# Performance work log

Hardware: AMD Instinct MI355X
Metric: run time of the kernel (lower is better)

The kernel has to match this reference:

```python
import jax, jax.numpy as jnp
import numpy as np

H = 16        # num_attention_heads
G = 16        # groups
SCALE_MIN = 0.95
SCALE_MAX = 1.05


def setup_inputs() -> dict:
    key = jax.random.key(0)
    ks = jax.random.split(key, 9)
    B, S, E = 2, 2048, 1024
    d = {
        'hidden_states': jax.random.normal(ks[0], (B, S, E), jnp.float32),
        'Wq': jax.random.normal(ks[1], (E, E), jnp.float32) * (E ** -0.5),
        'bq': jax.random.normal(ks[2], (E,), jnp.float32) * 0.02,
        'Wk': jax.random.normal(ks[3], (E, E), jnp.float32) * (E ** -0.5),
        'bk': jax.random.normal(ks[4], (E,), jnp.float32) * 0.02,
        'Wv': jax.random.normal(ks[5], (E, E), jnp.float32) * (E ** -0.5),
        'bv': jax.random.normal(ks[6], (E,), jnp.float32) * 0.02,
        'Ws': jax.random.normal(ks[7], (H * G, E), jnp.float32) * (E ** -0.5),
        'bs': jax.random.normal(ks[8], (H * G,), jnp.float32) * 0.02,
    }
    return d


def _shape_heads(x, B, S):
    # [B,S,h*D] -> [B,h,S,D]
    return x.reshape(B, S, H, -1).transpose(0, 2, 1, 3)


def reference(hidden_states, Wq, bq, Wk, bk, Wv, bv, Ws, bs):
    B, S, E = hidden_states.shape
    D = E // H            # head dim = 64
    gd = D // G           # group dim = 4

    Q = _shape_heads(hidden_states @ Wq.T + bq, B, S)   # [B,h,S,D]
    K = _shape_heads(hidden_states @ Wk.T + bk, B, S)
    V = _shape_heads(hidden_states @ Wv.T + bv, B, S)

    # groupwise dynamic scales, narrow sigmoid range
    s_logits = hidden_states @ Ws.T + bs                 # [B,S,h*g]
    s = jax.nn.sigmoid(s_logits) * (SCALE_MAX - SCALE_MIN) + SCALE_MIN
    s = s.reshape(B, S, H, G).transpose(0, 2, 1, 3)      # [B,h,S,g]
    s = jnp.repeat(s, gd, axis=-1)                       # [B,h,S,D]

    Q = Q * s  # apply_to='q'

    scores = jnp.einsum('bhsd,bhtd->bhst', Q, K) / jnp.sqrt(jnp.float32(D))
    probs = jax.nn.softmax(scores, axis=-1)
    ctx = jnp.einsum('bhst,bhtd->bhsd', probs, V)        # [B,h,S,D]
    ctx = ctx.transpose(0, 2, 1, 3).reshape(B, S, H * D)
    return ctx
```

## Files before the change

### kernel.cpp

```cpp
#include <hip/hip_runtime.h>

typedef short bf16x8 __attribute__((ext_vector_type(8)));
typedef short bf16x4 __attribute__((ext_vector_type(4)));
typedef float f32x4 __attribute__((ext_vector_type(4)));

__device__ inline float bf2f(ushort u) {
    unsigned v = ((unsigned)u) << 16;
    return __builtin_bit_cast(float, v);
}
__device__ inline ushort f2bf(float f) {
    unsigned u = __builtin_bit_cast(unsigned, f);
    u += 0x7fffu + ((u >> 16) & 1u);
    return (ushort)(u >> 16);
}
__device__ inline void async_load16(const ushort* g, ushort* l) {
    __builtin_amdgcn_global_load_lds((const __attribute__((address_space(1))) void*)g,
                                     (__attribute__((address_space(3))) void*)l, 16, 0, 0);
}
__device__ inline f32x4 mfma16(bf16x4 a, bf16x4 b, f32x4 c) {
#if __has_builtin(__builtin_amdgcn_mfma_f32_16x16x16_bf16)
    return __builtin_amdgcn_mfma_f32_16x16x16_bf16(a, b, c, 0, 0, 0);
#else
    return __builtin_amdgcn_mfma_f32_16x16x16bf16_1k(a, b, c, 0, 0, 0);
#endif
}

__global__ void cast_all(const float* __restrict__ hs, const float* __restrict__ Wq,
                         const float* __restrict__ Wk, const float* __restrict__ Wv,
                         const float* __restrict__ Ws,
                         ushort* __restrict__ dhs, ushort* __restrict__ dWq,
                         ushort* __restrict__ dWk, ushort* __restrict__ dWv,
                         ushort* __restrict__ dWs)
{
    int bid = blockIdx.x;
    const float* src; ushort* dst; int off;
    if (bid < 2048)      { src = hs; dst = dhs; off = bid; }
    else if (bid < 2560) { src = Wq; dst = dWq; off = bid - 2048; }
    else if (bid < 3072) { src = Wk; dst = dWk; off = bid - 2560; }
    else if (bid < 3584) { src = Wv; dst = dWv; off = bid - 3072; }
    else                 { src = Ws; dst = dWs; off = bid - 3584; }
    int i = (off * 256 + threadIdx.x) * 8;
    float4 a = *(const float4*)(src + i);
    float4 b = *(const float4*)(src + i + 4);
    union { ushort u[8]; float4 v; } o;
    o.u[0] = f2bf(a.x); o.u[1] = f2bf(a.y); o.u[2] = f2bf(a.z); o.u[3] = f2bf(a.w);
    o.u[4] = f2bf(b.x); o.u[5] = f2bf(b.y); o.u[6] = f2bf(b.z); o.u[7] = f2bf(b.w);
    *(float4*)(dst + i) = o.v;
}

__launch_bounds__(256, 4)
__global__ void fused_qkvs(const ushort* __restrict__ X,
                           const ushort* __restrict__ Wq, const ushort* __restrict__ Wk,
                           const ushort* __restrict__ Wv, const ushort* __restrict__ Ws,
                           const float* __restrict__ bq, const float* __restrict__ bk,
                           const float* __restrict__ bv, const float* __restrict__ bs,
                           ushort* __restrict__ Qb, ushort* __restrict__ Kb,
                           ushort* __restrict__ VtG, float* __restrict__ sb)
{
    __shared__ __align__(16) ushort Sm[128 * 136];
    ushort* As = Sm;
    ushort* Bs = Sm + 128 * 64;

    const int tid = threadIdx.x, w = tid >> 6, lane = tid & 63;
    const int l15 = lane & 15, quad = lane >> 4;
    const int lrow = lane >> 3;
    const int gchunk = ((lane & 7) ^ lrow) * 8;

    const int wid = blockIdx.x;
    const int r8 = wid & 7, jj = wid >> 3;
    const int by = (jj & 3) * 8 + r8;
    const int xb = jj >> 2;
    const int m0 = by * 128;

    const ushort* W; const float* bias; int n0, mode;
    if (xb < 8)       { W = Wq; bias = bq; n0 = xb * 128;        mode = 1; }
    else if (xb < 16) { W = Wk; bias = bk; n0 = (xb - 8) * 128;  mode = 0; }
    else if (xb < 24) { W = Wv; bias = bv; n0 = (xb - 16) * 128; mode = 2; }
    else              { W = Ws; bias = bs; n0 = (xb - 24) * 128; mode = 3; }

    const int wm = (w >> 1) * 64, wn = (w & 1) * 64;

    f32x4 acc[4][4];
    for (int i = 0; i < 4; i++) for (int j = 0; j < 4; j++) acc[i][j] = (f32x4){0.f, 0.f, 0.f, 0.f};

    for (int k0 = 0; k0 < 1024; k0 += 64) {
        __syncthreads();
        for (int c = 0; c < 4; ++c) {
            int r = w * 32 + c * 8;
            async_load16(&X[(size_t)(m0 + r + lrow) * 1024 + k0 + gchunk], &As[r * 64]);
            async_load16(&W[(size_t)(n0 + r + lrow) * 1024 + k0 + gchunk], &Bs[r * 64]);
        }
        __syncthreads();
        for (int kk = 0; kk < 64; kk += 32) {
            const int csw = quad + (kk >> 3);
            bf16x8 a[4], b[4];
            for (int i = 0; i < 4; i++)
                a[i] = *(const bf16x8*)&As[(wm + i * 16 + l15) * 64 + ((csw ^ (l15 & 7)) * 8)];
            for (int j = 0; j < 4; j++)
                b[j] = *(const bf16x8*)&Bs[(wn + j * 16 + l15) * 64 + ((csw ^ (l15 & 7)) * 8)];
            for (int i = 0; i < 4; i++)
                for (int j = 0; j < 4; j++)
                    acc[i][j] = __builtin_amdgcn_mfma_f32_16x16x32_bf16(a[i], b[j], acc[i][j], 0, 0, 0);
        }
    }

    const float QSCALE = 0.125f * 1.44269504f;

    if (mode == 3) {
        for (int i = 0; i < 4; i++)
            for (int j = 0; j < 4; j++) {
                int gn = n0 + wn + j * 16 + l15;
                float bv_ = bias[gn];
                for (int r = 0; r < 4; r++) {
                    int gm = m0 + wm + i * 16 + quad * 4 + r;
                    float v = acc[i][j][r] + bv_;
                    float sg = __builtin_amdgcn_rcpf(1.0f + __builtin_amdgcn_exp2f(-v * 1.44269504f));
                    sb[(size_t)gm * 256 + gn] = sg * 0.1f + 0.95f;
                }
            }
        return;
    }

    __syncthreads();

    if (mode == 2) {
        for (int i = 0; i < 4; i++)
            for (int j = 0; j < 4; j++) {
                int gnl = wn + j * 16 + l15;
                float bv_ = bias[n0 + gnl];
                ushort4 pk;
                pk.x = f2bf(acc[i][j][0] + bv_);
                pk.y = f2bf(acc[i][j][1] + bv_);
                pk.z = f2bf(acc[i][j][2] + bv_);
                pk.w = f2bf(acc[i][j][3] + bv_);
                *(ushort4*)&Sm[gnl * 136 + wm + i * 16 + quad * 4] = pk;
            }
        __syncthreads();
        const int bb = m0 >> 11, sloc = m0 & 2047;
        for (int it = 0; it < 8; ++it) {
            int d = (tid >> 4) + it * 16;
            int s8 = (tid & 15) * 8;
            float4 v = *(float4*)&Sm[d * 136 + s8];
            int h = (n0 + d) >> 6, dd = d & 63;
            *(float4*)&VtG[(size_t)(bb * 16 + h) * 131072 + (size_t)dd * 2048 + sloc + s8] = v;
        }
    } else {
        for (int i = 0; i < 4; i++)
            for (int j = 0; j < 4; j++) {
                int gnl = wn + j * 16 + l15;
                float bv_ = bias[n0 + gnl];
                for (int r = 0; r < 4; r++) {
                    float v = acc[i][j][r] + bv_;
                    if (mode == 1) v *= QSCALE;
                    Sm[(wm + i * 16 + quad * 4 + r) * 136 + gnl] = f2bf(v);
                }
            }
        __syncthreads();
        ushort* dst = (mode == 1) ? Qb : Kb;
        for (int it = 0; it < 8; ++it) {
            int row = (tid >> 4) + it * 16, c = (tid & 15) * 8;
            *(float4*)&dst[(size_t)(m0 + row) * 1024 + n0 + c] = *(float4*)&Sm[row * 136 + c];
        }
    }
}

__launch_bounds__(256, 4)
__global__ void attn_kernel(const ushort* __restrict__ Q, const ushort* __restrict__ K,
                            const ushort* __restrict__ Vt, const float* __restrict__ sb,
                            float* __restrict__ out)
{
    __shared__ __align__(16) ushort SmA[4 * 4096];
    ushort* Ks0 = SmA;
    ushort* Ks1 = SmA + 4096;
    ushort* Vs0 = SmA + 8192;
    ushort* Vs1 = SmA + 12288;
    ushort* Qs  = SmA + 4096;

    const int tid = threadIdx.x, w = tid >> 6, lane = tid & 63;
    const int l15 = lane & 15, quad = lane >> 4;
    const int lrow = lane >> 3;
    const int gchunk = ((lane & 7) ^ lrow) * 8;

    const int wid = blockIdx.x;
    const int r8 = wid & 7, jj = wid >> 3;
    const int bh = (jj & 3) * 8 + r8;
    const int qx = jj >> 2;
    const int b = bh >> 4, h = bh & 15;
    const int q0 = qx * 64;
    const size_t rowbase = (size_t)b * 2048;
    const int cbase = h * 64;

    const ushort* kg = K + (rowbase + w * 16 + lrow) * 1024 + cbase + gchunk;
    const ushort* vg = Vt + (size_t)bh * 131072 + (size_t)(w * 16 + lrow) * 2048 + gchunk;

    for (int c = 0; c < 2; ++c) {
        async_load16(kg + c * 8192,  Ks0 + w * 1024 + c * 512);
        async_load16(vg + c * 16384, Vs0 + w * 1024 + c * 512);
    }

    for (int it = 0; it < 2; ++it) {
        int l = tid + it * 256;
        int r = l >> 3, ch = l & 7;
        int c = ch * 8;
        union { float4 f; ushort u[8]; } uu, oo;
        uu.f = *(const float4*)&Q[(rowbase + q0 + r) * 1024 + cbase + c];
        const float* sp = &sb[(rowbase + q0 + r) * 256 + ((cbase + c) >> 2)];
        float s0 = sp[0], s1 = sp[1];
        for (int j = 0; j < 4; j++) oo.u[j] = f2bf(bf2f(uu.u[j]) * s0);
        for (int j = 4; j < 8; j++) oo.u[j] = f2bf(bf2f(uu.u[j]) * s1);
        *(float4*)&Qs[r * 64 + ((ch ^ (r & 7)) * 8)] = oo.f;
    }
    __syncthreads();

    bf16x8 aq[2];
    for (int kk2 = 0; kk2 < 2; kk2++)
        aq[kk2] = *(const bf16x8*)&Qs[(w * 16 + l15) * 64
                                      + (((kk2 * 4 + quad) ^ (l15 & 7)) * 8)];

    int kvoff[2][4];
    for (int kk2 = 0; kk2 < 2; kk2++)
        for (int nt = 0; nt < 4; nt++)
            kvoff[kk2][nt] = (nt * 16 + l15) * 64 + (((quad + kk2 * 4) ^ (l15 & 7)) * 8);
    int vaddr[4];
    for (int kt2 = 0; kt2 < 4; kt2++)
        vaddr[kt2] = l15 * 64 + (quad & 1) * 4
                   + (((kt2 * 2 + (quad >> 1)) ^ (l15 & 7)) * 8);

    const bf16x4 vones4 = {0x3F80, 0x3F80, 0x3F80, 0x3F80};

    f32x4 osum = (f32x4){0.f, 0.f, 0.f, 0.f};
    f32x4 o[4];
    for (int nt = 0; nt < 4; nt++) o[nt] = (f32x4){0.f, 0.f, 0.f, 0.f};
    const f32x4 z4 = (f32x4){0.f, 0.f, 0.f, 0.f};

#define ATTN_STEP(KC, VC, KN, VN, KT, PREFETCH)                                                         \
    {                                                                                                   \
        __syncthreads();                  \
        if (PREFETCH) {                                                                                 \
            const int nk = (KT) + 1;                                                                    \
            for (int c = 0; c < 2; ++c) {                                                               \
                async_load16(kg + nk * 65536 + c * 8192, KN + w * 1024 + c * 512);                      \
                async_load16(vg + nk * 64 + c * 16384,   VN + w * 1024 + c * 512);                      \
            }                                                                                           \
        }                                                                                               \
        bf16x8 kb[2][4];                                                                                \
        for (int kk2 = 0; kk2 < 2; kk2++)                                                               \
            for (int nt = 0; nt < 4; nt++)                                                              \
                kb[kk2][nt] = *(const bf16x8*)&KC[kvoff[kk2][nt]];                                      \
        bf16x4 vb4[4][4];                                                                               \
        _Pragma("unroll")                                                                               \
        for (int kt2 = 0; kt2 < 4; kt2++)                                                               \
            _Pragma("unroll")                                                                           \
            for (int nt = 0; nt < 4; nt++)                                                              \
                vb4[kt2][nt] = *(const bf16x4*)&VC[vaddr[kt2] + nt * 1024];                             \
                                                     \
        f32x4 st[4];                                                                                    \
        _Pragma("unroll")                                                                               \
        for (int kt2 = 0; kt2 < 4; kt2++) {                                                             \
            st[kt2] = __builtin_amdgcn_mfma_f32_16x16x32_bf16(kb[0][kt2], aq[0], z4, 0, 0, 0);          \
            st[kt2] = __builtin_amdgcn_mfma_f32_16x16x32_bf16(kb[1][kt2], aq[1], st[kt2], 0, 0, 0);     \
        }                                                                                               \
                           \
        unsigned du0[4], du1[4];                                                                        \
        _Pragma("unroll")                                                                               \
        for (int kt2 = 0; kt2 < 4; kt2++) {                                                             \
            float p0 = __builtin_amdgcn_exp2f(st[kt2][0]);                                              \
            float p1 = __builtin_amdgcn_exp2f(st[kt2][1]);                                              \
            float p2 = __builtin_amdgcn_exp2f(st[kt2][2]);                                              \
            float p3 = __builtin_amdgcn_exp2f(st[kt2][3]);                                              \
            du0[kt2] = __builtin_amdgcn_perm(__builtin_bit_cast(unsigned, p1) + 0x8000u,                \
                                             __builtin_bit_cast(unsigned, p0) + 0x8000u,                \
                                             0x07060302u);                                              \
            du1[kt2] = __builtin_amdgcn_perm(__builtin_bit_cast(unsigned, p3) + 0x8000u,                \
                                             __builtin_bit_cast(unsigned, p2) + 0x8000u,                \
                                             0x07060302u);                                              \
        }                                                                                               \
                              \
        _Pragma("unroll")                                                                               \
        for (int kt2 = 0; kt2 < 4; kt2++) {                                                             \
            union { unsigned u[2]; bf16x4 v; } af;                                                      \
            af.u[0] = du0[kt2]; af.u[1] = du1[kt2];                                                     \
            osum = mfma16(af.v, vones4, osum);                                                          \
            _Pragma("unroll")                                                                           \
            for (int nt = 0; nt < 4; nt++)                                                              \
                o[nt] = mfma16(af.v, vb4[kt2][nt], o[nt]);                                              \
        }                                                                                               \
    }

    for (int kt = 0; kt < 32; kt += 2) {
        ATTN_STEP(Ks0, Vs0, Ks1, Vs1, kt, 1);
        ATTN_STEP(Ks1, Vs1, Ks0, Vs0, kt + 1, (kt + 2 < 32));
    }
#undef ATTN_STEP

    for (int r = 0; r < 4; r++) {
        float iv = __builtin_amdgcn_rcpf(osum[r]);
        int q = q0 + w * 16 + quad * 4 + r;
        size_t base = (rowbase + q) * 1024 + cbase;
        for (int nt = 0; nt < 4; nt++)
            out[base + nt * 16 + l15] = o[nt][r] * iv;
    }
}

extern "C" void kernel_launch(void* const* d_in, const int* in_sizes, int n_in,
                              void* d_out, int out_size, void* d_ws, size_t ws_size,
                              hipStream_t stream) {
    const float* hs = (const float*)d_in[0];
    const float* Wq = (const float*)d_in[1];
    const float* bq = (const float*)d_in[2];
    const float* Wk = (const float*)d_in[3];
    const float* bk = (const float*)d_in[4];
    const float* Wv = (const float*)d_in[5];
    const float* bv = (const float*)d_in[6];
    const float* Ws = (const float*)d_in[7];
    const float* bs = (const float*)d_in[8];
    float* outp = (float*)d_out;

    char* ws = (char*)d_ws;
    ushort* Qb    = (ushort*)(ws);
    ushort* Kb    = (ushort*)(ws + 8388608);
    ushort* VtG   = (ushort*)(ws + 16777216);
    float*  sb    = (float* )(ws + 25165824);
    ushort* hs_bf = (ushort*)(ws + 29360128);
    ushort* Wq_bf = (ushort*)(ws + 37748736);
    ushort* Wk_bf = (ushort*)(ws + 39845888);
    ushort* Wv_bf = (ushort*)(ws + 41943040);
    ushort* Ws_bf = (ushort*)(ws + 44040192);

    cast_all<<<dim3(3712), dim3(256), 0, stream>>>(hs, Wq, Wk, Wv, Ws,
                                                   hs_bf, Wq_bf, Wk_bf, Wv_bf, Ws_bf);
    fused_qkvs<<<dim3(832), dim3(256), 0, stream>>>(hs_bf, Wq_bf, Wk_bf, Wv_bf, Ws_bf,
                                                    bq, bk, bv, bs, Qb, Kb, VtG, sb);
    attn_kernel<<<dim3(1024), dim3(256), 0, stream>>>(Qb, Kb, VtG, sb, outp);
}
```

Before: 177.3 us.

## Double query rows per attention block to reuse K/V tiles across two M-tiles

Each attention block now handles 128 query rows instead of 64, with each wave computing two 16-row M-tiles that share the same K and V fragments loaded from LDS. The grid halves to 512 blocks, Q gets its own LDS region, and launch bounds drop to 2 blocks per SM. This aims to cut K/V global and LDS traffic per query row. The cost is more registers, fewer blocks, and lower occupancy, which could hurt latency hiding and load balance across CUs.

```diff
diff --git a/kernel.cpp b/kernel.cpp
--- a/kernel.cpp
+++ b/kernel.cpp
@@ -164,17 +164,17 @@
     }
 }
 
-__launch_bounds__(256, 4)
+__launch_bounds__(256, 2)
 __global__ void attn_kernel(const ushort* __restrict__ Q, const ushort* __restrict__ K,
                             const ushort* __restrict__ Vt, const float* __restrict__ sb,
                             float* __restrict__ out)
 {
-    __shared__ __align__(16) ushort SmA[4 * 4096];
+    __shared__ __align__(16) ushort SmA[4 * 4096 + 8192];
     ushort* Ks0 = SmA;
     ushort* Ks1 = SmA + 4096;
     ushort* Vs0 = SmA + 8192;
     ushort* Vs1 = SmA + 12288;
-    ushort* Qs  = SmA + 4096;
+    ushort* Qs  = SmA + 16384;
 
     const int tid = threadIdx.x, w = tid >> 6, lane = tid & 63;
     const int l15 = lane & 15, quad = lane >> 4;
@@ -186,7 +186,7 @@
     const int bh = (jj & 3) * 8 + r8;
     const int qx = jj >> 2;
     const int b = bh >> 4, h = bh & 15;
-    const int q0 = qx * 64;
+    const int q0 = qx * 128;
     const size_t rowbase = (size_t)b * 2048;
     const int cbase = h * 64;
 
@@ -198,7 +198,7 @@
         async_load16(vg + c * 16384, Vs0 + w * 1024 + c * 512);
     }
 
-    for (int it = 0; it < 2; ++it) {
+    for (int it = 0; it < 4; ++it) {
         int l = tid + it * 256;
         int r = l >> 3, ch = l & 7;
         int c = ch * 8;
@@ -212,10 +212,11 @@
     }
     __syncthreads();
 
-    bf16x8 aq[2];
-    for (int kk2 = 0; kk2 < 2; kk2++)
-        aq[kk2] = *(const bf16x8*)&Qs[(w * 16 + l15) * 64
-                                      + (((kk2 * 4 + quad) ^ (l15 & 7)) * 8)];
+    bf16x8 aq[2][2];
+    for (int mt = 0; mt < 2; mt++)
+        for (int kk2 = 0; kk2 < 2; kk2++)
+            aq[mt][kk2] = *(const bf16x8*)&Qs[(w * 32 + mt * 16 + l15) * 64
+                                              + (((kk2 * 4 + quad) ^ (l15 & 7)) * 8)];
 
     int kvoff[2][4];
     for (int kk2 = 0; kk2 < 2; kk2++)
@@ -228,9 +229,12 @@
 
     const bf16x4 vones4 = {0x3F80, 0x3F80, 0x3F80, 0x3F80};
 
-    f32x4 osum = (f32x4){0.f, 0.f, 0.f, 0.f};
-    f32x4 o[4];
-    for (int nt = 0; nt < 4; nt++) o[nt] = (f32x4){0.f, 0.f, 0.f, 0.f};
+    f32x4 osum[2];
+    f32x4 o[2][4];
+    for (int mt = 0; mt < 2; mt++) {
+        osum[mt] = (f32x4){0.f, 0.f, 0.f, 0.f};
+        for (int nt = 0; nt < 4; nt++) o[mt][nt] = (f32x4){0.f, 0.f, 0.f, 0.f};
+    }
     const f32x4 z4 = (f32x4){0.f, 0.f, 0.f, 0.f};
 
 #define ATTN_STEP(KC, VC, KN, VN, KT, PREFETCH)                                                         \
@@ -253,37 +257,41 @@
             _Pragma("unroll")                                                                           \
             for (int nt = 0; nt < 4; nt++)                                                              \
                 vb4[kt2][nt] = *(const bf16x4*)&VC[vaddr[kt2] + nt * 1024];                             \
+        _Pragma("unroll")                                                                               \
+        for (int mt = 0; mt < 2; mt++) {                                                                \
                                                      \
-        f32x4 st[4];                                                                                    \
-        _Pragma("unroll")                                                                               \
-        for (int kt2 = 0; kt2 < 4; kt2++) {                                                             \
-            st[kt2] = __builtin_amdgcn_mfma_f32_16x16x32_bf16(kb[0][kt2], aq[0], z4, 0, 0, 0);          \
-            st[kt2] = __builtin_amdgcn_mfma_f32_16x16x32_bf16(kb[1][kt2], aq[1], st[kt2], 0, 0, 0);     \
-        }                                                                                               \
+            f32x4 st[4];                                                                                \
+            _Pragma("unroll")                                                                           \
+            for (int kt2 = 0; kt2 < 4; kt2++) {                                                         \
+                st[kt2] = __builtin_amdgcn_mfma_f32_16x16x32_bf16(kb[0][kt2], aq[mt][0], z4, 0, 0, 0);  \
+                st[kt2] = __builtin_amdgcn_mfma_f32_16x16x32_bf16(kb[1][kt2], aq[mt][1], st[kt2],       \
+                                                                  0, 0, 0);                             \
+            }                                                                                           \
                            \
-        unsigned du0[4], du1[4];                                                                        \
-        _Pragma("unroll")                                                                               \
-        for (int kt2 = 0; kt2 < 4; kt2++) {                                                             \
-            float p0 = __builtin_amdgcn_exp2f(st[kt2][0]);                                              \
-            float p1 = __builtin_amdgcn_exp2f(st[kt2][1]);                                              \
-            float p2 = __builtin_amdgcn_exp2f(st[kt2][2]);                                              \
-            float p3 = __builtin_amdgcn_exp2f(st[kt2][3]);                                              \
-            du0[kt2] = __builtin_amdgcn_perm(__builtin_bit_cast(unsigned, p1) + 0x8000u,                \
-                                             __builtin_bit_cast(unsigned, p0) + 0x8000u,                \
-                                             0x07060302u);                                              \
-            du1[kt2] = __builtin_amdgcn_perm(__builtin_bit_cast(unsigned, p3) + 0x8000u,                \
-                                             __builtin_bit_cast(unsigned, p2) + 0x8000u,                \
-                                             0x07060302u);                                              \
-        }                                                                                               \
+            unsigned du0[4], du1[4];                                                                    \
+            _Pragma("unroll")                                                                           \
+            for (int kt2 = 0; kt2 < 4; kt2++) {                                                         \
+                float p0 = __builtin_amdgcn_exp2f(st[kt2][0]);                                          \
+                float p1 = __builtin_amdgcn_exp2f(st[kt2][1]);                                          \
+                float p2 = __builtin_amdgcn_exp2f(st[kt2][2]);                                          \
+                float p3 = __builtin_amdgcn_exp2f(st[kt2][3]);                                          \
+                du0[kt2] = __builtin_amdgcn_perm(__builtin_bit_cast(unsigned, p1) + 0x8000u,            \
+                                                 __builtin_bit_cast(unsigned, p0) + 0x8000u,            \
+                                                 0x07060302u);                                          \
+                du1[kt2] = __builtin_amdgcn_perm(__builtin_bit_cast(unsigned, p3) + 0x8000u,            \
+                                                 __builtin_bit_cast(unsigned, p2) + 0x8000u,            \
+                                                 0x07060302u);                                          \
+            }                                                                                           \
                               \
-        _Pragma("unroll")                                                                               \
-        for (int kt2 = 0; kt2 < 4; kt2++) {                                                             \
-            union { unsigned u[2]; bf16x4 v; } af;                                                      \
-            af.u[0] = du0[kt2]; af.u[1] = du1[kt2];                                                     \
-            osum = mfma16(af.v, vones4, osum);                                                          \
             _Pragma("unroll")                                                                           \
-            for (int nt = 0; nt < 4; nt++)                                                              \
-                o[nt] = mfma16(af.v, vb4[kt2][nt], o[nt]);                                              \
+            for (int kt2 = 0; kt2 < 4; kt2++) {                                                         \
+                union { unsigned u[2]; bf16x4 v; } af;                                                  \
+                af.u[0] = du0[kt2]; af.u[1] = du1[kt2];                                                 \
+                osum[mt] = mfma16(af.v, vones4, osum[mt]);                                              \
+                _Pragma("unroll")                                                                       \
+                for (int nt = 0; nt < 4; nt++)                                                          \
+                    o[mt][nt] = mfma16(af.v, vb4[kt2][nt], o[mt][nt]);                                  \
+            }                                                                                           \
         }                                                                                               \
     }
 
@@ -293,12 +301,14 @@
     }
 #undef ATTN_STEP
 
-    for (int r = 0; r < 4; r++) {
-        float iv = __builtin_amdgcn_rcpf(osum[r]);
-        int q = q0 + w * 16 + quad * 4 + r;
-        size_t base = (rowbase + q) * 1024 + cbase;
-        for (int nt = 0; nt < 4; nt++)
-            out[base + nt * 16 + l15] = o[nt][r] * iv;
+    for (int mt = 0; mt < 2; mt++) {
+        for (int r = 0; r < 4; r++) {
+            float iv = __builtin_amdgcn_rcpf(osum[mt][r]);
+            int q = q0 + w * 32 + mt * 16 + quad * 4 + r;
+            size_t base = (rowbase + q) * 1024 + cbase;
+            for (int nt = 0; nt < 4; nt++)
+                out[base + nt * 16 + l15] = o[mt][nt][r] * iv;
+        }
     }
 }
 
@@ -331,5 +341,5 @@
                                                    hs_bf, Wq_bf, Wk_bf, Wv_bf, Ws_bf);
     fused_qkvs<<<dim3(832), dim3(256), 0, stream>>>(hs_bf, Wq_bf, Wk_bf, Wv_bf, Ws_bf,
                                                     bq, bk, bv, bs, Qb, Kb, VtG, sb);
-    attn_kernel<<<dim3(1024), dim3(256), 0, stream>>>(Qb, Kb, VtG, sb, outp);
-}
+    attn_kernel<<<dim3(512), dim3(256), 0, stream>>>(Qb, Kb, VtG, sb, outp);
+}
```

Result: faster. 169.3 us (-4.5%).
